# Performance work log

Measured on AMD Instinct MI355X. Metric: run time of the kernel, lower is better.

## Reference

```python
import jax, jax.numpy as jnp
import numpy as np

B, C, H, W = 4, 64, 64, 64

def setup_inputs() -> dict:
    key = jax.random.key(0)
    ks = jax.random.split(key, 9)
    return {
        "x": jax.random.normal(ks[0], (B, C, H, W), dtype=jnp.float32),
        "Wq": jax.random.normal(ks[1], (C, C), dtype=jnp.float32) * (1.0 / np.sqrt(C)),
        "bq": jax.random.normal(ks[2], (C,), dtype=jnp.float32) * 0.02,
        "Wk": jax.random.normal(ks[3], (C, C), dtype=jnp.float32) * (1.0 / np.sqrt(C)),
        "bk": jax.random.normal(ks[4], (C,), dtype=jnp.float32) * 0.02,
        "Wv": jax.random.normal(ks[5], (C, C), dtype=jnp.float32) * (1.0 / np.sqrt(C)),
        "bv": jax.random.normal(ks[6], (C,), dtype=jnp.float32) * 0.02,
        "rel_h": jax.random.normal(ks[7], (1, C, H, 1), dtype=jnp.float32),
        "rel_w": jax.random.normal(ks[8], (1, C, 1, W), dtype=jnp.float32),
    }

def reference(x, Wq, bq, Wk, bk, Wv, bv, rel_h, rel_w):
    b, c, h, w = x.shape
    n = h * w
    xf = x.reshape(b, c, n)                                  # [B,C,N]
    # 1x1 convs == channel-wise linear maps (weight [out,in])
    q = jnp.einsum('oc,bcn->bno', Wq, xf) + bq               # [B,N,C]
    k = jnp.einsum('oc,bcn->bon', Wk, xf) + bk[:, None]      # [B,C,N]
    v = jnp.einsum('oc,bcn->bon', Wv, xf) + bv[:, None]      # [B,C,N]
    energy = jnp.einsum('bnc,bcm->bnm', q, k)                # content term [B,N,N]
    pos = (rel_h + rel_w).reshape(c, n)                      # [C,N]
    energy = energy + jnp.einsum('bnc,cm->bnm', q, pos)      # add positional bias
    attn = jax.nn.softmax(energy, axis=-1)                   # [B,N,N]
    # out[b,c,n] = sum_m v[b,c,m] * attn[b,n,m]  (bmm with attention^T)
    out = jnp.einsum('bcm,bnm->bcn', v, attn)
    return out.reshape(b, c, h, w)
```

## Files before the change

kernel.cpp:

```cpp
#include <hip/hip_runtime.h>
#include <math.h>

#define NPOS 4096
#define NB   4
#define NROW (NB * NPOS)
#define LOG2E 1.44269504088896f

typedef _Float16 f16;
typedef f16 f16x4 __attribute__((ext_vector_type(4)));
typedef f16 f16x8 __attribute__((ext_vector_type(8)));
typedef float f32x4 __attribute__((ext_vector_type(4)));

#define LDW 72

__global__ __launch_bounds__(256) void qkv_proj(
    const float* __restrict__ x,
    const float* __restrict__ Wq, const float* __restrict__ bq,
    const float* __restrict__ Wk, const float* __restrict__ bk,
    const float* __restrict__ Wv, const float* __restrict__ bv,
    const float* __restrict__ rel_h, const float* __restrict__ rel_w,
    f16* __restrict__ qh, f16* __restrict__ kh, f16* __restrict__ vh)
{
    __shared__ f16 Xs[64 * LDW];
    __shared__ f16 Ws[192 * LDW];

    const int tid = threadIdx.x;
    const int b   = blockIdx.x >> 6;
    const int n0  = (blockIdx.x & 63) << 6;

    #pragma unroll
    for (int k = 0; k < 12; ++k) {
        int idx  = tid + k * 256;
        int orow = idx >> 4;
        int cseg = (idx & 15) << 2;
        int mat  = orow >> 6;
        int o    = orow & 63;
        const float* wsrc = (mat == 0) ? Wq : ((mat == 1) ? Wk : Wv);
        float4 v = *(const float4*)(wsrc + o * 64 + cseg);
        f16x4 h; h[0] = (f16)v.x; h[1] = (f16)v.y; h[2] = (f16)v.z; h[3] = (f16)v.w;
        *(f16x4*)(&Ws[orow * LDW + cseg]) = h;
    }
    #pragma unroll
    for (int k = 0; k < 4; ++k) {
        int idx  = tid + k * 256;
        int c    = idx >> 4;
        int nseg = (idx & 15) << 2;
        float4 v = *(const float4*)(x + ((size_t)(b * 64 + c)) * NPOS + n0 + nseg);
        Xs[(nseg + 0) * LDW + c] = (f16)v.x;
        Xs[(nseg + 1) * LDW + c] = (f16)v.y;
        Xs[(nseg + 2) * LDW + c] = (f16)v.z;
        Xs[(nseg + 3) * LDW + c] = (f16)v.w;
    }
    __syncthreads();

    const int wave = tid >> 6;
    const int lane = tid & 63;
    const int quad = lane >> 4;
    const int l16  = lane & 15;

    const f16x8 a0 = *(const f16x8*)(&Xs[(wave * 16 + l16) * LDW + quad * 8]);
    const f16x8 a1 = *(const f16x8*)(&Xs[(wave * 16 + l16) * LDW + 32 + quad * 8]);

    f32x4 acc[12];
    #pragma unroll
    for (int t = 0; t < 12; ++t) {
        f32x4 c0 = {0, 0, 0, 0};
        f16x8 b0 = *(const f16x8*)(&Ws[(t * 16 + l16) * LDW + quad * 8]);
        f16x8 b1 = *(const f16x8*)(&Ws[(t * 16 + l16) * LDW + 32 + quad * 8]);
        c0 = __builtin_amdgcn_mfma_f32_16x16x32_f16(a0, b0, c0, 0, 0, 0);
        c0 = __builtin_amdgcn_mfma_f32_16x16x32_f16(a1, b1, c0, 0, 0, 0);
        acc[t] = c0;
    }

    #pragma unroll
    for (int r = 0; r < 4; ++r) {
        int n = n0 + wave * 16 + quad * 4 + r;
        int h = n >> 6, w = n & 63;
        #pragma unroll
        for (int t = 0; t < 4; ++t) {
            int o = t * 16 + l16;
            qh[((size_t)b * NPOS + n) * 64 + o] = (f16)((acc[t][r] + bq[o]) * LOG2E);
        }
        #pragma unroll
        for (int t = 4; t < 8; ++t) {
            int o = (t - 4) * 16 + l16;
            kh[((size_t)b * NPOS + n) * 64 + o] =
                (f16)(acc[t][r] + bk[o] + rel_h[o * 64 + h] + rel_w[o * 64 + w]);
        }
    }

    __syncthreads();
    #pragma unroll
    for (int r = 0; r < 4; ++r) {
        int nl = wave * 16 + quad * 4 + r;
        #pragma unroll
        for (int t = 8; t < 12; ++t) {
            int o = (t - 8) * 16 + l16;
            Xs[o * LDW + nl] = (f16)(acc[t][r] + bv[o]);
        }
    }
    __syncthreads();
    {
        int o  = tid >> 2;
        int ns = (tid & 3) << 4;
        f16* dst = vh + ((size_t)(b * 64 + o)) * NPOS + n0 + ns;
        *(f16x8*)(dst)     = *(const f16x8*)(&Xs[o * LDW + ns]);
        *(f16x8*)(dst + 8) = *(const f16x8*)(&Xs[o * LDW + ns + 8]);
    }
}

#define LDP 72

__global__ __launch_bounds__(256, 8) void attn(
    const f16* __restrict__ qh, const f16* __restrict__ kh,
    const f16* __restrict__ vh,
    f16* __restrict__ Op, float* __restrict__ Mp, float* __restrict__ Lp,
    int split, int mchunk)
{
    __shared__ f16 Ks[64 * LDP];
    __shared__ f16 Vt[64 * LDP];

    const int tid  = threadIdx.x;
    const int wave = tid >> 6;
    const int lane = tid & 63;
    const int quad = lane >> 4;
    const int l16  = lane & 15;
    const int s    = blockIdx.x % split;
    const int tile = blockIdx.x / split;
    const int b    = tile >> 6;
    const int n0   = (tile & 63) << 6;

    const f16* qbase = qh + ((size_t)b * NPOS + n0 + wave * 16 + l16) * 64;
    const f16x8 bq0 = *(const f16x8*)(qbase + quad * 8);
    const f16x8 bq1 = *(const f16x8*)(qbase + 32 + quad * 8);

    f32x4 O[4] = {{0,0,0,0},{0,0,0,0},{0,0,0,0},{0,0,0,0}};
    float m_i = -1e30f, l_i = 0.f;

    const int srow = tid >> 2;
    const int sseg = (tid & 3) * 16;
    const f16* kb = kh + (size_t)b * NPOS * 64;
    const f16* vb = vh + (size_t)b * 64 * NPOS;

    const int m_begin = s * mchunk;
    for (int m0 = m_begin; m0 < m_begin + mchunk; m0 += 64) {
        const f16* ksrc = kb + (size_t)(m0 + srow) * 64 + sseg;
        *(f16x8*)(&Ks[srow * LDP + sseg])     = *(const f16x8*)(ksrc);
        *(f16x8*)(&Ks[srow * LDP + sseg + 8]) = *(const f16x8*)(ksrc + 8);
        const f16* vsrc = vb + (size_t)srow * NPOS + m0 + sseg;
        *(f16x8*)(&Vt[srow * LDP + sseg])     = *(const f16x8*)(vsrc);
        *(f16x8*)(&Vt[srow * LDP + sseg + 8]) = *(const f16x8*)(vsrc + 8);
        __syncthreads();

        f32x4 S[4];
        #pragma unroll
        for (int t = 0; t < 4; ++t) {
            f32x4 acc = {0, 0, 0, 0};
            f16x8 ak0 = *(const f16x8*)(&Ks[(t * 16 + l16) * LDP + quad * 8]);
            f16x8 ak1 = *(const f16x8*)(&Ks[(t * 16 + l16) * LDP + 32 + quad * 8]);
            acc = __builtin_amdgcn_mfma_f32_16x16x32_f16(ak0, bq0, acc, 0, 0, 0);
            acc = __builtin_amdgcn_mfma_f32_16x16x32_f16(ak1, bq1, acc, 0, 0, 0);
            S[t] = acc;
        }

        float mx = S[0][0];
        #pragma unroll
        for (int t = 0; t < 4; ++t)
            #pragma unroll
            for (int r = 0; r < 4; ++r) mx = fmaxf(mx, S[t][r]);
        mx = fmaxf(mx, __shfl_xor(mx, 16));
        mx = fmaxf(mx, __shfl_xor(mx, 32));
        float mnew  = fmaxf(m_i, mx);
        float alpha = __builtin_amdgcn_exp2f(m_i - mnew);
        float p[4][4];
        float rs = 0.f;
        #pragma unroll
        for (int t = 0; t < 4; ++t)
            #pragma unroll
            for (int r = 0; r < 4; ++r) {
                float e = __builtin_amdgcn_exp2f(S[t][r] - mnew);
                p[t][r] = e;
                rs += e;
            }
        rs += __shfl_xor(rs, 16);
        rs += __shfl_xor(rs, 32);
        m_i = mnew;
        l_i = l_i * alpha + rs;

        #pragma unroll
        for (int r = 0; r < 4; ++r) {
            float av = __shfl(alpha, quad * 20 + r);
            O[0][r] *= av; O[1][r] *= av; O[2][r] *= av; O[3][r] *= av;
        }

        f16x4 pa[4];
        #pragma unroll
        for (int t = 0; t < 4; ++t) {
            f16x4 a;
            a[0] = (f16)p[t][0]; a[1] = (f16)p[t][1];
            a[2] = (f16)p[t][2]; a[3] = (f16)p[t][3];
            pa[t] = a;
        }

        #pragma unroll
        for (int u = 0; u < 4; ++u) {
            #pragma unroll
            for (int t = 0; t < 4; ++t) {
                f16x4 bf = *(const f16x4*)(&Vt[(u * 16 + l16) * LDP + t * 16 + quad * 4]);
                O[u] = __builtin_amdgcn_mfma_f32_16x16x16f16(pa[t], bf, O[u], 0, 0, 0);
            }
        }
        __syncthreads();
    }

    #pragma unroll
    for (int r = 0; r < 4; ++r) {
        float lr  = __shfl(l_i, quad * 20 + r);
        float inv = 1.f / lr;
        int n = n0 + wave * 16 + quad * 4 + r;
        size_t row = (size_t)b * NPOS + n;
        #pragma unroll
        for (int u = 0; u < 4; ++u)
            Op[((size_t)s * NROW + row) * 64 + u * 16 + l16] = (f16)(O[u][r] * inv);
    }
    if (lane < 16) {
        size_t row = (size_t)b * NPOS + n0 + wave * 16 + l16;
        Mp[(size_t)s * NROW + row] = m_i;
        Lp[(size_t)s * NROW + row] = l_i;
    }
}

__global__ __launch_bounds__(256) void combine(
    const f16* __restrict__ Op, const float* __restrict__ Mp,
    const float* __restrict__ Lp, float* __restrict__ out, int split)
{
    __shared__ float Ot[64 * 68];

    const int tid = threadIdx.x;
    const int b   = blockIdx.x >> 6;
    const int n0  = (blockIdx.x & 63) << 6;

    {
        int nl = tid >> 2;
        int cs = (tid & 3) << 4;
        size_t row = (size_t)b * NPOS + n0 + nl;

        float M = -1e30f;
        for (int s2 = 0; s2 < split; ++s2)
            M = fmaxf(M, Mp[(size_t)s2 * NROW + row]);

        float L = 0.f;
        float val[16];
        #pragma unroll
        for (int j = 0; j < 16; ++j) val[j] = 0.f;
        for (int s2 = 0; s2 < split; ++s2) {
            float w = Lp[(size_t)s2 * NROW + row] *
                      __builtin_amdgcn_exp2f(Mp[(size_t)s2 * NROW + row] - M);
            L += w;
            const f16* op = Op + ((size_t)s2 * NROW + row) * 64 + cs;
            f16x8 o0 = *(const f16x8*)(op);
            f16x8 o1 = *(const f16x8*)(op + 8);
            #pragma unroll
            for (int j = 0; j < 8; ++j) {
                val[j]     += w * (float)o0[j];
                val[8 + j] += w * (float)o1[j];
            }
        }
        float invL = 1.f / L;
        #pragma unroll
        for (int k = 0; k < 4; ++k) {
            float4 v4 = { val[4*k] * invL, val[4*k+1] * invL,
                          val[4*k+2] * invL, val[4*k+3] * invL };
            *(float4*)(&Ot[nl * 68 + cs + 4 * k]) = v4;
        }
    }
    __syncthreads();
    {
        int c  = tid >> 2;
        int ns = (tid & 3) << 4;
        float* dst = out + ((size_t)(b * 64 + c)) * NPOS + n0 + ns;
        #pragma unroll
        for (int k = 0; k < 4; ++k) {
            float4 v4 = { Ot[(ns + 4*k + 0) * 68 + c], Ot[(ns + 4*k + 1) * 68 + c],
                          Ot[(ns + 4*k + 2) * 68 + c], Ot[(ns + 4*k + 3) * 68 + c] };
            *(float4*)(&dst[4 * k]) = v4;
        }
    }
}

extern "C" void kernel_launch(void* const* d_in, const int* in_sizes, int n_in,
                              void* d_out, int out_size, void* d_ws, size_t ws_size,
                              hipStream_t stream) {
    const float* x     = (const float*)d_in[0];
    const float* Wq    = (const float*)d_in[1];
    const float* bq    = (const float*)d_in[2];
    const float* Wk    = (const float*)d_in[3];
    const float* bk    = (const float*)d_in[4];
    const float* Wv    = (const float*)d_in[5];
    const float* bv    = (const float*)d_in[6];
    const float* rel_h = (const float*)d_in[7];
    const float* rel_w = (const float*)d_in[8];
    float* out = (float*)d_out;

    const size_t qkv_elems = (size_t)NROW * 64;
    int split = 8;
    {
        size_t need = 3 * qkv_elems * sizeof(f16)
                    + (size_t)split * NROW * 64 * sizeof(f16)
                    + 2 * (size_t)split * NROW * sizeof(float);
        if (ws_size < need) split = 4;
    }
    const int mchunk = NPOS / split;

    f16* qh = (f16*)d_ws;
    f16* kh = qh + qkv_elems;
    f16* vh = kh + qkv_elems;
    f16* Op = vh + qkv_elems;
    float* Mp = (float*)(Op + (size_t)split * NROW * 64);
    float* Lp = Mp + (size_t)split * NROW;

    qkv_proj<<<NB * (NPOS / 64), 256, 0, stream>>>(x, Wq, bq, Wk, bk, Wv, bv,
                                                   rel_h, rel_w, qh, kh, vh);
    attn<<<NB * (NPOS / 64) * split, 256, 0, stream>>>(qh, kh, vh, Op, Mp, Lp,
                                                       split, mchunk);
    combine<<<NB * (NPOS / 64), 256, 0, stream>>>(Op, Mp, Lp, out, split);
}
```

Before: 128.8 us.

## Fuse split-KV combine into attention, widen KV tile, add lazy rescale

The combine kernel is folded into the attention kernel: the last split block for each tile, found with an atomic counter, does the merge, so one launch and a pass over the partials go away. The attention KV tile grows from 64 to 128 keys per iteration, and occupancy hints drop from 8 to 4 blocks. The output rescale is skipped when no running max increases. The QKV projection now uses 16-position blocks with 4x more blocks, so each wave computes 3 output tiles. These changes add a memset and threadfence/atomic overhead, and the larger shared-memory footprint may lower occupancy.

```diff
diff --git a/kernel.cpp b/kernel.cpp
--- a/kernel.cpp
+++ b/kernel.cpp
@@ -21,12 +21,13 @@
     const float* __restrict__ rel_h, const float* __restrict__ rel_w,
     f16* __restrict__ qh, f16* __restrict__ kh, f16* __restrict__ vh)
 {
-    __shared__ f16 Xs[64 * LDW];
-    __shared__ f16 Ws[192 * LDW];
+    __shared__ __align__(16) f16 Ws[192 * LDW];
+    __shared__ __align__(16) f16 Xs[16 * LDW];
+    __shared__ __align__(16) f16 Vs[64 * 20];
 
     const int tid = threadIdx.x;
-    const int b   = blockIdx.x >> 6;
-    const int n0  = (blockIdx.x & 63) << 6;
+    const int b   = blockIdx.x >> 8;
+    const int n0  = (blockIdx.x & 255) << 4;
 
     #pragma unroll
     for (int k = 0; k < 12; ++k) {
@@ -40,16 +41,14 @@
         f16x4 h; h[0] = (f16)v.x; h[1] = (f16)v.y; h[2] = (f16)v.z; h[3] = (f16)v.w;
         *(f16x4*)(&Ws[orow * LDW + cseg]) = h;
     }
-    #pragma unroll
-    for (int k = 0; k < 4; ++k) {
-        int idx  = tid + k * 256;
-        int c    = idx >> 4;
-        int nseg = (idx & 15) << 2;
-        float4 v = *(const float4*)(x + ((size_t)(b * 64 + c)) * NPOS + n0 + nseg);
-        Xs[(nseg + 0) * LDW + c] = (f16)v.x;
-        Xs[(nseg + 1) * LDW + c] = (f16)v.y;
-        Xs[(nseg + 2) * LDW + c] = (f16)v.z;
-        Xs[(nseg + 3) * LDW + c] = (f16)v.w;
+    {
+        int c  = tid >> 2;
+        int ns = (tid & 3) << 2;
+        float4 v = *(const float4*)(x + ((size_t)(b * 64 + c)) * NPOS + n0 + ns);
+        Xs[(ns + 0) * LDW + c] = (f16)v.x;
+        Xs[(ns + 1) * LDW + c] = (f16)v.y;
+        Xs[(ns + 2) * LDW + c] = (f16)v.z;
+        Xs[(ns + 3) * LDW + c] = (f16)v.w;
     }
     __syncthreads();
 
@@ -58,67 +57,73 @@
     const int quad = lane >> 4;
     const int l16  = lane & 15;
 
-    const f16x8 a0 = *(const f16x8*)(&Xs[(wave * 16 + l16) * LDW + quad * 8]);
-    const f16x8 a1 = *(const f16x8*)(&Xs[(wave * 16 + l16) * LDW + 32 + quad * 8]);
-
-    f32x4 acc[12];
+    const f16x8 a0 = *(const f16x8*)(&Xs[l16 * LDW + quad * 8]);
+    const f16x8 a1 = *(const f16x8*)(&Xs[l16 * LDW + 32 + quad * 8]);
+
+    f32x4 acc[3];
+    const int t0 = wave * 3;
     #pragma unroll
-    for (int t = 0; t < 12; ++t) {
+    for (int i = 0; i < 3; ++i) {
+        int t = t0 + i;
         f32x4 c0 = {0, 0, 0, 0};
         f16x8 b0 = *(const f16x8*)(&Ws[(t * 16 + l16) * LDW + quad * 8]);
         f16x8 b1 = *(const f16x8*)(&Ws[(t * 16 + l16) * LDW + 32 + quad * 8]);
         c0 = __builtin_amdgcn_mfma_f32_16x16x32_f16(a0, b0, c0, 0, 0, 0);
         c0 = __builtin_amdgcn_mfma_f32_16x16x32_f16(a1, b1, c0, 0, 0, 0);
-        acc[t] = c0;
+        acc[i] = c0;
     }
 
     #pragma unroll
-    for (int r = 0; r < 4; ++r) {
-        int n = n0 + wave * 16 + quad * 4 + r;
-        int h = n >> 6, w = n & 63;
-        #pragma unroll
-        for (int t = 0; t < 4; ++t) {
+    for (int i = 0; i < 3; ++i) {
+        int t = t0 + i;
+        if (t < 4) {
             int o = t * 16 + l16;
-            qh[((size_t)b * NPOS + n) * 64 + o] = (f16)((acc[t][r] + bq[o]) * LOG2E);
-        }
-        #pragma unroll
-        for (int t = 4; t < 8; ++t) {
+            float bb = bq[o];
+            #pragma unroll
+            for (int r = 0; r < 4; ++r) {
+                size_t n = (size_t)b * NPOS + n0 + quad * 4 + r;
+                qh[n * 64 + o] = (f16)((acc[i][r] + bb) * LOG2E);
+            }
+        } else if (t < 8) {
             int o = (t - 4) * 16 + l16;
-            kh[((size_t)b * NPOS + n) * 64 + o] =
-                (f16)(acc[t][r] + bk[o] + rel_h[o * 64 + h] + rel_w[o * 64 + w]);
-        }
-    }
-
-    __syncthreads();
-    #pragma unroll
-    for (int r = 0; r < 4; ++r) {
-        int nl = wave * 16 + quad * 4 + r;
-        #pragma unroll
-        for (int t = 8; t < 12; ++t) {
+            int h = n0 >> 6;
+            int wbase = n0 & 63;
+            float bb = bk[o] + rel_h[o * 64 + h];
+            #pragma unroll
+            for (int r = 0; r < 4; ++r) {
+                size_t n = (size_t)b * NPOS + n0 + quad * 4 + r;
+                kh[n * 64 + o] = (f16)(acc[i][r] + bb + rel_w[o * 64 + wbase + quad * 4 + r]);
+            }
+        } else {
             int o = (t - 8) * 16 + l16;
-            Xs[o * LDW + nl] = (f16)(acc[t][r] + bv[o]);
-        }
-    }
-    __syncthreads();
-    {
-        int o  = tid >> 2;
-        int ns = (tid & 3) << 4;
-        f16* dst = vh + ((size_t)(b * 64 + o)) * NPOS + n0 + ns;
-        *(f16x8*)(dst)     = *(const f16x8*)(&Xs[o * LDW + ns]);
-        *(f16x8*)(dst + 8) = *(const f16x8*)(&Xs[o * LDW + ns + 8]);
+            float bb = bv[o];
+            #pragma unroll
+            for (int r = 0; r < 4; ++r)
+                Vs[o * 20 + quad * 4 + r] = (f16)(acc[i][r] + bb);
+        }
+    }
+    __syncthreads();
+    {
+        int c  = tid >> 2;
+        int ns = (tid & 3) << 2;
+        f16x4 vv = *(const f16x4*)(&Vs[c * 20 + ns]);
+        *(f16x4*)(vh + ((size_t)(b * 64 + c)) * NPOS + n0 + ns) = vv;
     }
 }
 
-#define LDP 72
-
-__global__ __launch_bounds__(256, 8) void attn(
+#define LDK 72
+#define LDV 136
+
+__global__ __launch_bounds__(256, 4) void attn(
     const f16* __restrict__ qh, const f16* __restrict__ kh,
     const f16* __restrict__ vh,
     f16* __restrict__ Op, float* __restrict__ Mp, float* __restrict__ Lp,
+    int* __restrict__ cnt, float* __restrict__ out,
     int split, int mchunk)
 {
-    __shared__ f16 Ks[64 * LDP];
-    __shared__ f16 Vt[64 * LDP];
+    __shared__ __align__(16) f16 Ks[128 * LDK];
+    __shared__ __align__(16) f16 Vt[64 * LDV];
+    __shared__ int lastFlag;
 
     const int tid  = threadIdx.x;
     const int wave = tid >> 6;
@@ -137,27 +142,31 @@
     f32x4 O[4] = {{0,0,0,0},{0,0,0,0},{0,0,0,0},{0,0,0,0}};
     float m_i = -1e30f, l_i = 0.f;
 
-    const int srow = tid >> 2;
-    const int sseg = (tid & 3) * 16;
+    const int krow = tid >> 1;
+    const int kseg = (tid & 1) * 32;
+    const int vrow = tid >> 2;
+    const int vseg = (tid & 3) * 32;
     const f16* kb = kh + (size_t)b * NPOS * 64;
     const f16* vb = vh + (size_t)b * 64 * NPOS;
 
     const int m_begin = s * mchunk;
-    for (int m0 = m_begin; m0 < m_begin + mchunk; m0 += 64) {
-        const f16* ksrc = kb + (size_t)(m0 + srow) * 64 + sseg;
-        *(f16x8*)(&Ks[srow * LDP + sseg])     = *(const f16x8*)(ksrc);
-        *(f16x8*)(&Ks[srow * LDP + sseg + 8]) = *(const f16x8*)(ksrc + 8);
-        const f16* vsrc = vb + (size_t)srow * NPOS + m0 + sseg;
-        *(f16x8*)(&Vt[srow * LDP + sseg])     = *(const f16x8*)(vsrc);
-        *(f16x8*)(&Vt[srow * LDP + sseg + 8]) = *(const f16x8*)(vsrc + 8);
+    for (int m0 = m_begin; m0 < m_begin + mchunk; m0 += 128) {
+        const f16* ks = kb + (size_t)(m0 + krow) * 64 + kseg;
+        #pragma unroll
+        for (int j = 0; j < 4; ++j)
+            *(f16x8*)(&Ks[krow * LDK + kseg + 8 * j]) = *(const f16x8*)(ks + 8 * j);
+        const f16* vs = vb + (size_t)vrow * NPOS + m0 + vseg;
+        #pragma unroll
+        for (int j = 0; j < 4; ++j)
+            *(f16x8*)(&Vt[vrow * LDV + vseg + 8 * j]) = *(const f16x8*)(vs + 8 * j);
         __syncthreads();
 
-        f32x4 S[4];
-        #pragma unroll
-        for (int t = 0; t < 4; ++t) {
+        f32x4 S[8];
+        #pragma unroll
+        for (int t = 0; t < 8; ++t) {
             f32x4 acc = {0, 0, 0, 0};
-            f16x8 ak0 = *(const f16x8*)(&Ks[(t * 16 + l16) * LDP + quad * 8]);
-            f16x8 ak1 = *(const f16x8*)(&Ks[(t * 16 + l16) * LDP + 32 + quad * 8]);
+            f16x8 ak0 = *(const f16x8*)(&Ks[(t * 16 + l16) * LDK + quad * 8]);
+            f16x8 ak1 = *(const f16x8*)(&Ks[(t * 16 + l16) * LDK + 32 + quad * 8]);
             acc = __builtin_amdgcn_mfma_f32_16x16x32_f16(ak0, bq0, acc, 0, 0, 0);
             acc = __builtin_amdgcn_mfma_f32_16x16x32_f16(ak1, bq1, acc, 0, 0, 0);
             S[t] = acc;
@@ -165,48 +174,46 @@
 
         float mx = S[0][0];
         #pragma unroll
-        for (int t = 0; t < 4; ++t)
+        for (int t = 0; t < 8; ++t)
             #pragma unroll
             for (int r = 0; r < 4; ++r) mx = fmaxf(mx, S[t][r]);
         mx = fmaxf(mx, __shfl_xor(mx, 16));
         mx = fmaxf(mx, __shfl_xor(mx, 32));
-        float mnew  = fmaxf(m_i, mx);
-        float alpha = __builtin_amdgcn_exp2f(m_i - mnew);
-        float p[4][4];
+
+        if (__any(mx > m_i)) {
+            float mnew  = fmaxf(m_i, mx);
+            float alpha = __builtin_amdgcn_exp2f(m_i - mnew);
+            m_i = mnew;
+            l_i *= alpha;
+            #pragma unroll
+            for (int r = 0; r < 4; ++r) {
+                float av = __shfl(alpha, quad * 20 + r);
+                O[0][r] *= av; O[1][r] *= av; O[2][r] *= av; O[3][r] *= av;
+            }
+        }
+
         float rs = 0.f;
-        #pragma unroll
-        for (int t = 0; t < 4; ++t)
+        f16x4 pa[8];
+        #pragma unroll
+        for (int t = 0; t < 8; ++t) {
+            f16x4 a;
             #pragma unroll
             for (int r = 0; r < 4; ++r) {
-                float e = __builtin_amdgcn_exp2f(S[t][r] - mnew);
-                p[t][r] = e;
+                float e = __builtin_amdgcn_exp2f(S[t][r] - m_i);
                 rs += e;
-            }
+                a[r] = (f16)e;
+            }
+            pa[t] = a;
+        }
         rs += __shfl_xor(rs, 16);
         rs += __shfl_xor(rs, 32);
-        m_i = mnew;
-        l_i = l_i * alpha + rs;
-
-        #pragma unroll
-        for (int r = 0; r < 4; ++r) {
-            float av = __shfl(alpha, quad * 20 + r);
-            O[0][r] *= av; O[1][r] *= av; O[2][r] *= av; O[3][r] *= av;
-        }
-
-        f16x4 pa[4];
-        #pragma unroll
-        for (int t = 0; t < 4; ++t) {
-            f16x4 a;
-            a[0] = (f16)p[t][0]; a[1] = (f16)p[t][1];
-            a[2] = (f16)p[t][2]; a[3] = (f16)p[t][3];
-            pa[t] = a;
-        }
+        l_i += rs;
 
         #pragma unroll
         for (int u = 0; u < 4; ++u) {
             #pragma unroll
-            for (int t = 0; t < 4; ++t) {
-                f16x4 bf = *(const f16x4*)(&Vt[(u * 16 + l16) * LDP + t * 16 + quad * 4]);
+            for (int t = 0; t < 8; ++t) {
+                f16x4 bf = *(const f16x4*)(&Vt[(u * 16 + l16) * LDV + t * 16 + quad * 4]);
                 O[u] = __builtin_amdgcn_mfma_f32_16x16x16f16(pa[t], bf, O[u], 0, 0, 0);
             }
         }
@@ -217,8 +224,7 @@
     for (int r = 0; r < 4; ++r) {
         float lr  = __shfl(l_i, quad * 20 + r);
         float inv = 1.f / lr;
-        int n = n0 + wave * 16 + quad * 4 + r;
-        size_t row = (size_t)b * NPOS + n;
+        size_t row = (size_t)b * NPOS + n0 + wave * 16 + quad * 4 + r;
         #pragma unroll
         for (int u = 0; u < 4; ++u)
             Op[((size_t)s * NROW + row) * 64 + u * 16 + l16] = (f16)(O[u][r] * inv);
@@ -228,18 +234,18 @@
         Mp[(size_t)s * NROW + row] = m_i;
         Lp[(size_t)s * NROW + row] = l_i;
     }
-}
-
-__global__ __launch_bounds__(256) void combine(
-    const f16* __restrict__ Op, const float* __restrict__ Mp,
-    const float* __restrict__ Lp, float* __restrict__ out, int split)
-{
-    __shared__ float Ot[64 * 68];
-
-    const int tid = threadIdx.x;
-    const int b   = blockIdx.x >> 6;
-    const int n0  = (blockIdx.x & 63) << 6;
-
+
+    __threadfence();
+    __syncthreads();
+    if (tid == 0) {
+        int old = atomicAdd(&cnt[tile], 1);
+        lastFlag = (old == split - 1);
+    }
+    __syncthreads();
+    if (!lastFlag) return;
+    __threadfence();
+
+    float* Ot = (float*)Ks;
     {
         int nl = tid >> 2;
         int cs = (tid & 3) << 4;
@@ -307,7 +313,8 @@
     {
         size_t need = 3 * qkv_elems * sizeof(f16)
                     + (size_t)split * NROW * 64 * sizeof(f16)
-                    + 2 * (size_t)split * NROW * sizeof(float);
+                    + 2 * (size_t)split * NROW * sizeof(float)
+                    + 256 * sizeof(int);
         if (ws_size < need) split = 4;
     }
     const int mchunk = NPOS / split;
@@ -318,10 +325,11 @@
     f16* Op = vh + qkv_elems;
     float* Mp = (float*)(Op + (size_t)split * NROW * 64);
     float* Lp = Mp + (size_t)split * NROW;
-
-    qkv_proj<<<NB * (NPOS / 64), 256, 0, stream>>>(x, Wq, bq, Wk, bk, Wv, bv,
+    int*  cnt = (int*)(Lp + (size_t)split * NROW);
+
+    hipMemsetAsync(cnt, 0, 256 * sizeof(int), stream);
+    qkv_proj<<<NB * (NPOS / 16), 256, 0, stream>>>(x, Wq, bq, Wk, bk, Wv, bv,
                                                    rel_h, rel_w, qh, kh, vh);
     attn<<<NB * (NPOS / 64) * split, 256, 0, stream>>>(qh, kh, vh, Op, Mp, Lp,
-                                                       split, mchunk);
-    combine<<<NB * (NPOS / 64), 256, 0, stream>>>(Op, Mp, Lp, out, split);
+                                                       cnt, out, split, mchunk);
 }
```

New measurement: 507.9 us. +294.5%, slower.
